# Kernel optimization log

Measured on AMD Instinct MI355X. Metric: run time of the kernel, lower is better.

Reference implementation:

```python
import jax, jax.numpy as jnp
import numpy as np

HEADS = 8
EPS = 1e-5


def setup_inputs() -> dict:
    key = jax.random.key(0)
    B, N, C = 32, 4096, 256
    headc = C // HEADS
    x = jax.random.normal(key, (B, N, C), dtype=jnp.float32)
    return {
        "x": x,
        "kln_weight": jnp.ones((HEADS, 1, headc), dtype=jnp.float32),
        "kln_bias": jnp.zeros((HEADS, 1, headc), dtype=jnp.float32),
        "vln_weight": jnp.ones((HEADS, 1, headc), dtype=jnp.float32),
        "vln_bias": jnp.zeros((HEADS, 1, headc), dtype=jnp.float32),
    }


def _ln(t, w, b, headc):
    # Faithful to the torch module: unbiased std (ddof=1), eps added to std (not var).
    m = jnp.mean(t, axis=-1, keepdims=True)
    d = t - m
    std = jnp.sqrt(jnp.sum(d * d, axis=-1, keepdims=True) / (headc - 1))
    return w * (d / (std + EPS)) + b


def reference(x, kln_weight, kln_bias, vln_weight, vln_bias):
    B, N, C = x.shape
    headc = C // HEADS
    # [B, H, N, D]
    qkv = x.reshape(B, N, HEADS, headc).transpose(0, 2, 1, 3)
    k = _ln(qkv, kln_weight, kln_bias, headc)
    v = _ln(qkv, vln_weight, vln_bias, headc)
    # k^T v : [B, H, D, D], scaled by 1/N
    kv = jnp.einsum("bhnd,bhne->bhde", k, v) / N
    # q (k^T v): [B, H, N, D]
    out = jnp.einsum("bhnd,bhde->bhne", qkv, kv)
    out = out.transpose(0, 2, 1, 3).reshape(B, N, C)
    return out + x
```

## Files before the change

kernel.cpp:

```cpp
#include <hip/hip_runtime.h>

#define H_ 8
#define D_ 32
#define B_ 32
#define N_ 4096
#define C_ 256
#define EPS_ 1e-5f

#define SLOT_ 1088

typedef __attribute__((ext_vector_type(8))) short bf16x8;
typedef __attribute__((ext_vector_type(4))) float f32x4;

__device__ __forceinline__ short f2bf(float f) {
    unsigned u = __builtin_bit_cast(unsigned, f);
    unsigned r = (u + 0x7FFFu + ((u >> 16) & 1u)) >> 16;
    return (short)r;
}
__device__ __forceinline__ float bf2f(short s) {
    return __builtin_bit_cast(float, ((unsigned)(unsigned short)s) << 16);
}

__device__ __forceinline__ int uidx(int r, int c) {
    return r * 40 + ((r >> 3) & 3) * 16 + c;
}

__global__ __launch_bounds__(256, 4)
void k1_skv(const float* __restrict__ x, float* __restrict__ Pws)
{
    __shared__ short ubuf[256 * 40 + 64];

    const int tid  = threadIdx.x;
    const int bh   = blockIdx.x >> 2;
    const int q4   = blockIdx.x & 3;
    const int b    = bh >> 3;
    const int h    = bh & 7;
    const int lane = tid & 63;
    const int wave = tid >> 6;
    const int g    = lane >> 4;
    const int cL   = lane & 15;

    f32x4 acc[2][2] = {};
    f32x4 tq[2] = {};

    bf16x8 ones;
    #pragma unroll
    for (int j = 0; j < 8; ++j) ones[j] = (short)0x3F80;

    const float* xbase = x + ((size_t)b * N_ + q4 * 1024 + tid) * C_ + h * D_;

    float4 xA[8], xB[8];
    #pragma unroll
    for (int c = 0; c < 8; ++c)
        xA[c] = reinterpret_cast<const float4*>(xbase)[c];

    auto body = [&](const float4 (&xr)[8], float4 (&nx)[8], int it, bool pf) {
        if (pf) {
            const float* p = xbase + (size_t)(it + 1) * 256 * C_;
            #pragma unroll
            for (int c = 0; c < 8; ++c)
                nx[c] = reinterpret_cast<const float4*>(p)[c];
        }

        float sum = 0.f, sq = 0.f;
        #pragma unroll
        for (int c = 0; c < 8; ++c) {
            const float4 a = xr[c];
            sum += a.x + a.y + a.z + a.w;
            sq = fmaf(a.x, a.x, fmaf(a.y, a.y, fmaf(a.z, a.z, fmaf(a.w, a.w, sq))));
        }
        const float m   = sum * (1.f / 32.f);
        const float ss  = fmaxf(sq - sum * m, 0.f);
        const float inv = 1.f / (sqrtf(ss * (1.f / 31.f)) + EPS_);

        {
            const int base = tid * 40 + ((tid >> 3) & 3) * 16;
            #pragma unroll
            for (int q = 0; q < 4; ++q) {
                const float4 a0 = xr[q * 2 + 0];
                const float4 a1 = xr[q * 2 + 1];
                bf16x8 wv;
                wv[0] = f2bf((a0.x - m) * inv); wv[1] = f2bf((a0.y - m) * inv);
                wv[2] = f2bf((a0.z - m) * inv); wv[3] = f2bf((a0.w - m) * inv);
                wv[4] = f2bf((a1.x - m) * inv); wv[5] = f2bf((a1.y - m) * inv);
                wv[6] = f2bf((a1.z - m) * inv); wv[7] = f2bf((a1.w - m) * inv);
                *reinterpret_cast<bf16x8*>(&ubuf[base + q * 8]) = wv;
            }
        }
        asm volatile("s_waitcnt lgkmcnt(0)" ::: "memory");

        #pragma unroll
        for (int ks = 0; ks < 2; ++ks) {
            const int R0 = wave * 64 + ks * 32 + 8 * g;
            bf16x8 F0, F1;
            #pragma unroll
            for (int j = 0; j < 8; ++j) {
                const int base = uidx(R0 + j, cL);
                F0[j] = ubuf[base];
                F1[j] = ubuf[base + 16];
            }
            tq[0] = __builtin_amdgcn_mfma_f32_16x16x32_bf16(ones, F0, tq[0], 0, 0, 0);
            tq[1] = __builtin_amdgcn_mfma_f32_16x16x32_bf16(ones, F1, tq[1], 0, 0, 0);
            acc[0][0] = __builtin_amdgcn_mfma_f32_16x16x32_bf16(F0, F0, acc[0][0], 0, 0, 0);
            acc[0][1] = __builtin_amdgcn_mfma_f32_16x16x32_bf16(F0, F1, acc[0][1], 0, 0, 0);
            acc[1][0] = __builtin_amdgcn_mfma_f32_16x16x32_bf16(F1, F0, acc[1][0], 0, 0, 0);
            acc[1][1] = __builtin_amdgcn_mfma_f32_16x16x32_bf16(F1, F1, acc[1][1], 0, 0, 0);
        }
    };

    body(xA, xB, 0, true);
    body(xB, xA, 1, true);
    body(xA, xB, 2, true);
    body(xB, xA, 3, false);

    __syncthreads();
    float* sred = reinterpret_cast<float*>(ubuf);
    {
        float* dst = sred + wave * 1024;
        #pragma unroll
        for (int ca = 0; ca < 2; ++ca)
            #pragma unroll
            for (int cb = 0; cb < 2; ++cb)
                #pragma unroll
                for (int r = 0; r < 4; ++r)
                    dst[(ca * 16 + g * 4 + r) * D_ + cb * 16 + cL] = acc[ca][cb][r];
    }
    if (lane < 16) {
        sred[4096 + wave * 32 + cL]      = tq[0][0];
        sred[4096 + wave * 32 + 16 + cL] = tq[1][0];
    }
    __syncthreads();

    float* slot = Pws + (size_t)blockIdx.x * SLOT_;
    {
        const float4 c0 = *reinterpret_cast<const float4*>(&sred[tid * 4]);
        const float4 c1 = *reinterpret_cast<const float4*>(&sred[1024 + tid * 4]);
        const float4 c2 = *reinterpret_cast<const float4*>(&sred[2048 + tid * 4]);
        const float4 c3 = *reinterpret_cast<const float4*>(&sred[3072 + tid * 4]);
        float4 o;
        o.x = c0.x + c1.x + c2.x + c3.x;
        o.y = c0.y + c1.y + c2.y + c3.y;
        o.z = c0.z + c1.z + c2.z + c3.z;
        o.w = c0.w + c1.w + c2.w + c3.w;
        *reinterpret_cast<float4*>(slot + tid * 4) = o;
    }
    if (tid < D_)
        slot[1024 + tid] = sred[4096 + tid] + sred[4096 + 32 + tid]
                         + sred[4096 + 64 + tid] + sred[4096 + 96 + tid];
}

__global__ __launch_bounds__(256, 4)
void k_red(const float* __restrict__ Pws,
           const float* __restrict__ kw, const float* __restrict__ kb,
           const float* __restrict__ vw, const float* __restrict__ vb,
           short* __restrict__ kvHi, short* __restrict__ kvLo)
{
    const int bh  = blockIdx.x;
    const int h   = bh & 7;
    const int tid = threadIdx.x;
    const int d   = tid >> 3;
    const int e0  = (tid & 7) * 4;

    const float* P0 = Pws + (size_t)(bh * 4 + 0) * SLOT_;
    const float* P1 = Pws + (size_t)(bh * 4 + 1) * SLOT_;
    const float* P2 = Pws + (size_t)(bh * 4 + 2) * SLOT_;
    const float* P3 = Pws + (size_t)(bh * 4 + 3) * SLOT_;
    const float invN = 1.f / (float)N_;

    const float4 s0 = *reinterpret_cast<const float4*>(P0 + d * D_ + e0);
    const float4 s1 = *reinterpret_cast<const float4*>(P1 + d * D_ + e0);
    const float4 s2 = *reinterpret_cast<const float4*>(P2 + d * D_ + e0);
    const float4 s3 = *reinterpret_cast<const float4*>(P3 + d * D_ + e0);
    float Sde[4] = { s0.x + s1.x + s2.x + s3.x, s0.y + s1.y + s2.y + s3.y,
                     s0.z + s1.z + s2.z + s3.z, s0.w + s1.w + s2.w + s3.w };

    const float Td  = P0[1024 + d] + P1[1024 + d] + P2[1024 + d] + P3[1024 + d];
    const float wkd = kw[h * D_ + d];
    const float bkd = kb[h * D_ + d];

    #pragma unroll
    for (int j = 0; j < 4; ++j) {
        const int e = e0 + j;
        const float Te  = P0[1024 + e] + P1[1024 + e] + P2[1024 + e] + P3[1024 + e];
        const float wve = vw[h * D_ + e];
        const float bve = vb[h * D_ + e];
        const float v = invN * (wkd * (wve * Sde[j] + bve * Td) + bkd * wve * Te)
                      + bkd * bve;
        const short hi = f2bf(v);
        const short lo = f2bf(v - bf2f(hi));
        const int hf  = e >> 4;
        const int l   = ((d >> 3) << 4) | (e & 15);
        const int idx = bh * 1024 + hf * 512 + l * 8 + (d & 7);
        kvHi[idx] = hi;
        kvLo[idx] = lo;
    }
}

__global__ __launch_bounds__(256, 2)
void k2_out(const float* __restrict__ x,
            const short* __restrict__ kvHi, const short* __restrict__ kvLo,
            float* __restrict__ out)
{
    __shared__ float xt[64][256];

    const int tid  = threadIdx.x;
    const int lane = tid & 63;
    const int w    = tid >> 6;
    const int g    = lane >> 4;
    const int cL   = lane & 15;
    const int r0   = blockIdx.x * 64;
    const int b    = blockIdx.x >> 6;
    const int wr   = w * 16;

    bf16x8 Bhi[16], Blo[16];
    #pragma unroll
    for (int h = 0; h < 8; ++h)
        #pragma unroll
        for (int hf = 0; hf < 2; ++hf) {
            const size_t off = (size_t)(b * H_ + h) * 1024 + hf * 512 + lane * 8;
            Bhi[h * 2 + hf] = *reinterpret_cast<const bf16x8*>(kvHi + off);
            Blo[h * 2 + hf] = *reinterpret_cast<const bf16x8*>(kvLo + off);
        }

    const float* gx = x + (size_t)(r0 + wr) * C_ + lane * 4;
    {
        float4 v[8];
        #pragma unroll
        for (int i = 0; i < 8; ++i)
            v[i] = *reinterpret_cast<const float4*>(gx + (size_t)i * C_);
        #pragma unroll
        for (int i = 0; i < 8; ++i)
            *reinterpret_cast<float4*>(&xt[wr + i][lane * 4]) = v[i];
        #pragma unroll
        for (int i = 0; i < 8; ++i)
            v[i] = *reinterpret_cast<const float4*>(gx + (size_t)(i + 8) * C_);
        #pragma unroll
        for (int i = 0; i < 8; ++i)
            *reinterpret_cast<float4*>(&xt[wr + 8 + i][lane * 4]) = v[i];
    }
    asm volatile("s_waitcnt lgkmcnt(0)" ::: "memory");
    __builtin_amdgcn_sched_barrier(0);

    const f32x4 zero = {0.f, 0.f, 0.f, 0.f};

    #pragma unroll
    for (int h = 0; h < 8; ++h) {
        const float4 a0 = *reinterpret_cast<const float4*>(&xt[wr + cL][h * 32 + 8 * g]);
        const float4 a1 = *reinterpret_cast<const float4*>(&xt[wr + cL][h * 32 + 8 * g + 4]);
        bf16x8 A;
        A[0] = f2bf(a0.x); A[1] = f2bf(a0.y); A[2] = f2bf(a0.z); A[3] = f2bf(a0.w);
        A[4] = f2bf(a1.x); A[5] = f2bf(a1.y); A[6] = f2bf(a1.z); A[7] = f2bf(a1.w);

        #pragma unroll
        for (int hf = 0; hf < 2; ++hf) {
            f32x4 Dv = __builtin_amdgcn_mfma_f32_16x16x32_bf16(A, Blo[h * 2 + hf], zero, 0, 0, 0);
            Dv = __builtin_amdgcn_mfma_f32_16x16x32_bf16(A, Bhi[h * 2 + hf], Dv, 0, 0, 0);
            const int col = h * 32 + hf * 16 + cL;
            #pragma unroll
            for (int r = 0; r < 4; ++r) {
                const int rr = wr + 4 * g + r;
                out[(size_t)(r0 + rr) * C_ + col] = Dv[r] + xt[rr][col];
            }
        }
    }
}

extern "C" void kernel_launch(void* const* d_in, const int* in_sizes, int n_in,
                              void* d_out, int out_size, void* d_ws, size_t ws_size,
                              hipStream_t stream)
{
    const float* x  = (const float*)d_in[0];
    const float* kw = (const float*)d_in[1];
    const float* kb = (const float*)d_in[2];
    const float* vw = (const float*)d_in[3];
    const float* vb = (const float*)d_in[4];
    float* outp = (float*)d_out;

    float* Pws  = (float*)d_ws;
    short* kvHi = (short*)(Pws + (size_t)1024 * SLOT_);
    short* kvLo = kvHi + (size_t)256 * 1024;

    k1_skv<<<dim3(B_ * H_ * 4), dim3(256), 0, stream>>>(x, Pws);
    k_red<<<dim3(B_ * H_), dim3(256), 0, stream>>>(Pws, kw, kb, vw, vb, kvHi, kvLo);
    k2_out<<<dim3(B_ * N_ / 64), dim3(256), 0, stream>>>(x, kvHi, kvLo, outp);
}
```

Measured before the change: 81.24 us.

## Fold residual into KV via identity, drop LDS staging in output kernel

Adds the identity matrix to the per-head KV matrix so the residual x is produced by the matmul itself, which lets the output kernel skip re-reading x for the add. The output kernel no longer stages x tiles in shared memory. It loads q and the KV fragments straight from global memory, software-pipelined two heads at a time, and swaps the MFMA operands so each lane writes a contiguous float4. Occupancy is raised to 4 blocks per SM. The cost is that the residual now passes through bf16 hi/lo precision on q, which may add error to the added x term.

```diff
diff --git a/kernel.cpp b/kernel.cpp
--- a/kernel.cpp
+++ b/kernel.cpp
@@ -184,8 +184,9 @@
         const float Te  = P0[1024 + e] + P1[1024 + e] + P2[1024 + e] + P3[1024 + e];
         const float wve = vw[h * D_ + e];
         const float bve = vb[h * D_ + e];
-        const float v = invN * (wkd * (wve * Sde[j] + bve * Td) + bkd * wve * Te)
-                      + bkd * bve;
+        float v = invN * (wkd * (wve * Sde[j] + bve * Td) + bkd * wve * Te)
+                + bkd * bve;
+        if (d == e) v += 1.0f;
         const short hi = f2bf(v);
         const short lo = f2bf(v - bf2f(hi));
         const int hf  = e >> 4;
@@ -196,73 +197,71 @@
     }
 }
 
-__global__ __launch_bounds__(256, 2)
+__global__ __launch_bounds__(256, 4)
 void k2_out(const float* __restrict__ x,
             const short* __restrict__ kvHi, const short* __restrict__ kvLo,
             float* __restrict__ out)
 {
-    __shared__ float xt[64][256];
-
     const int tid  = threadIdx.x;
     const int lane = tid & 63;
     const int w    = tid >> 6;
     const int g    = lane >> 4;
     const int cL   = lane & 15;
-    const int r0   = blockIdx.x * 64;
     const int b    = blockIdx.x >> 6;
-    const int wr   = w * 16;
-
-    bf16x8 Bhi[16], Blo[16];
-    #pragma unroll
-    for (int h = 0; h < 8; ++h)
-        #pragma unroll
-        for (int hf = 0; hf < 2; ++hf) {
-            const size_t off = (size_t)(b * H_ + h) * 1024 + hf * 512 + lane * 8;
-            Bhi[h * 2 + hf] = *reinterpret_cast<const bf16x8*>(kvHi + off);
-            Blo[h * 2 + hf] = *reinterpret_cast<const bf16x8*>(kvLo + off);
-        }
-
-    const float* gx = x + (size_t)(r0 + wr) * C_ + lane * 4;
-    {
-        float4 v[8];
-        #pragma unroll
-        for (int i = 0; i < 8; ++i)
-            v[i] = *reinterpret_cast<const float4*>(gx + (size_t)i * C_);
-        #pragma unroll
-        for (int i = 0; i < 8; ++i)
-            *reinterpret_cast<float4*>(&xt[wr + i][lane * 4]) = v[i];
-        #pragma unroll
-        for (int i = 0; i < 8; ++i)
-            v[i] = *reinterpret_cast<const float4*>(gx + (size_t)(i + 8) * C_);
-        #pragma unroll
-        for (int i = 0; i < 8; ++i)
-            *reinterpret_cast<float4*>(&xt[wr + 8 + i][lane * 4]) = v[i];
-    }
-    asm volatile("s_waitcnt lgkmcnt(0)" ::: "memory");
-    __builtin_amdgcn_sched_barrier(0);
+    const int row  = blockIdx.x * 64 + w * 16 + cL;
+
+    const float* xr   = x + (size_t)row * C_;
+    float*       orow = out + (size_t)row * C_;
+    const size_t fb   = (size_t)(b * H_) * 1024 + lane * 8;
 
     const f32x4 zero = {0.f, 0.f, 0.f, 0.f};
 
-    #pragma unroll
-    for (int h = 0; h < 8; ++h) {
-        const float4 a0 = *reinterpret_cast<const float4*>(&xt[wr + cL][h * 32 + 8 * g]);
-        const float4 a1 = *reinterpret_cast<const float4*>(&xt[wr + cL][h * 32 + 8 * g + 4]);
-        bf16x8 A;
-        A[0] = f2bf(a0.x); A[1] = f2bf(a0.y); A[2] = f2bf(a0.z); A[3] = f2bf(a0.w);
-        A[4] = f2bf(a1.x); A[5] = f2bf(a1.y); A[6] = f2bf(a1.z); A[7] = f2bf(a1.w);
-
-        #pragma unroll
-        for (int hf = 0; hf < 2; ++hf) {
-            f32x4 Dv = __builtin_amdgcn_mfma_f32_16x16x32_bf16(A, Blo[h * 2 + hf], zero, 0, 0, 0);
-            Dv = __builtin_amdgcn_mfma_f32_16x16x32_bf16(A, Bhi[h * 2 + hf], Dv, 0, 0, 0);
-            const int col = h * 32 + hf * 16 + cL;
-            #pragma unroll
-            for (int r = 0; r < 4; ++r) {
-                const int rr = wr + 4 * g + r;
-                out[(size_t)(r0 + rr) * C_ + col] = Dv[r] + xt[rr][col];
-            }
-        }
-    }
+    bf16x8 hA0, lA0, hA1, lA1, hB0, lB0, hB1, lB1;
+    float4 qA0, qA1, qB0, qB1;
+
+#define LOADH(H, h0, l0, h1, l1, q0, q1)                                      \
+    h0 = *reinterpret_cast<const bf16x8*>(kvHi + fb + (H) * 1024);            \
+    l0 = *reinterpret_cast<const bf16x8*>(kvLo + fb + (H) * 1024);            \
+    h1 = *reinterpret_cast<const bf16x8*>(kvHi + fb + (H) * 1024 + 512);      \
+    l1 = *reinterpret_cast<const bf16x8*>(kvLo + fb + (H) * 1024 + 512);      \
+    q0 = *reinterpret_cast<const float4*>(xr + (H) * 32 + 8 * g);             \
+    q1 = *reinterpret_cast<const float4*>(xr + (H) * 32 + 8 * g + 4);
+
+#define COMPUTE(H, h0, l0, h1, l1, q0, q1)                                    \
+    {                                                                         \
+        bf16x8 Qb;                                                            \
+        Qb[0] = f2bf(q0.x); Qb[1] = f2bf(q0.y);                               \
+        Qb[2] = f2bf(q0.z); Qb[3] = f2bf(q0.w);                               \
+        Qb[4] = f2bf(q1.x); Qb[5] = f2bf(q1.y);                               \
+        Qb[6] = f2bf(q1.z); Qb[7] = f2bf(q1.w);                               \
+        f32x4 Dv;                                                             \
+        Dv = __builtin_amdgcn_mfma_f32_16x16x32_bf16(l0, Qb, zero, 0, 0, 0);  \
+        Dv = __builtin_amdgcn_mfma_f32_16x16x32_bf16(h0, Qb, Dv,   0, 0, 0);  \
+        *reinterpret_cast<f32x4*>(orow + (H) * 32 + 4 * g) = Dv;              \
+        Dv = __builtin_amdgcn_mfma_f32_16x16x32_bf16(l1, Qb, zero, 0, 0, 0);  \
+        Dv = __builtin_amdgcn_mfma_f32_16x16x32_bf16(h1, Qb, Dv,   0, 0, 0);  \
+        *reinterpret_cast<f32x4*>(orow + (H) * 32 + 16 + 4 * g) = Dv;         \
+    }
+
+    LOADH(0, hA0, lA0, hA1, lA1, qA0, qA1)
+    LOADH(1, hB0, lB0, hB1, lB1, qB0, qB1)
+    COMPUTE(0, hA0, lA0, hA1, lA1, qA0, qA1)
+    LOADH(2, hA0, lA0, hA1, lA1, qA0, qA1)
+    COMPUTE(1, hB0, lB0, hB1, lB1, qB0, qB1)
+    LOADH(3, hB0, lB0, hB1, lB1, qB0, qB1)
+    COMPUTE(2, hA0, lA0, hA1, lA1, qA0, qA1)
+    LOADH(4, hA0, lA0, hA1, lA1, qA0, qA1)
+    COMPUTE(3, hB0, lB0, hB1, lB1, qB0, qB1)
+    LOADH(5, hB0, lB0, hB1, lB1, qB0, qB1)
+    COMPUTE(4, hA0, lA0, hA1, lA1, qA0, qA1)
+    LOADH(6, hA0, lA0, hA1, lA1, qA0, qA1)
+    COMPUTE(5, hB0, lB0, hB1, lB1, qB0, qB1)
+    LOADH(7, hB0, lB0, hB1, lB1, qB0, qB1)
+    COMPUTE(6, hA0, lA0, hA1, lA1, qA0, qA1)
+    COMPUTE(7, hB0, lB0, hB1, lB1, qB0, qB1)
+
+#undef LOADH
+#undef COMPUTE
 }
 
 extern "C" void kernel_launch(void* const* d_in, const int* in_sizes, int n_in,
```

After: 84.50 us. 1.04x slower.

## Cache normalized rows in bf16 and fold the residual into kv via identity

Applied to the files above, without the earlier changes.

The first kernel now also writes each row's normalized values as bf16, plus its mean and std, to a global workspace. The reduction kernel adds the identity to kv, so q·kv + q becomes q·(kv+I), and it stores the column sums of that matrix. The output kernel rebuilds the result as sdev·(u·kv') + mean·colsum, so it reads half-size bf16 data instead of fp32 x and stages kv in LDS. In exchange the first kernel writes an extra intermediate, so total memory traffic may not drop. The residual now passes through bf16-rounded values, which loses accuracy, and the output stores are now per-row 16-byte chunks instead of coalesced row writes.

```diff
diff --git a/kernel.cpp b/kernel.cpp
--- a/kernel.cpp
+++ b/kernel.cpp
@@ -26,7 +26,8 @@
 }
 
 __global__ __launch_bounds__(256, 4)
-void k1_skv(const float* __restrict__ x, float* __restrict__ Pws)
+void k1_skv(const float* __restrict__ x, float* __restrict__ Pws,
+            short* __restrict__ ug, float2* __restrict__ msg)
 {
     __shared__ short ubuf[256 * 40 + 64];
 
@@ -69,10 +70,13 @@
             sum += a.x + a.y + a.z + a.w;
             sq = fmaf(a.x, a.x, fmaf(a.y, a.y, fmaf(a.z, a.z, fmaf(a.w, a.w, sq))));
         }
-        const float m   = sum * (1.f / 32.f);
-        const float ss  = fmaxf(sq - sum * m, 0.f);
-        const float inv = 1.f / (sqrtf(ss * (1.f / 31.f)) + EPS_);
-
+        const float m    = sum * (1.f / 32.f);
+        const float ss   = fmaxf(sq - sum * m, 0.f);
+        const float sdev = sqrtf(ss * (1.f / 31.f)) + EPS_;
+        const float inv  = 1.0f / sdev;
+
+        const size_t nrow = (size_t)bh * N_ + (size_t)q4 * 1024 + it * 256 + tid;
+        short* up = ug + nrow * 32;
         {
             const int base = tid * 40 + ((tid >> 3) & 3) * 16;
             #pragma unroll
@@ -85,8 +89,10 @@
                 wv[4] = f2bf((a1.x - m) * inv); wv[5] = f2bf((a1.y - m) * inv);
                 wv[6] = f2bf((a1.z - m) * inv); wv[7] = f2bf((a1.w - m) * inv);
                 *reinterpret_cast<bf16x8*>(&ubuf[base + q * 8]) = wv;
+                *reinterpret_cast<bf16x8*>(up + q * 8) = wv;
             }
         }
+        msg[nrow] = make_float2(m, sdev);
         asm volatile("s_waitcnt lgkmcnt(0)" ::: "memory");
 
         #pragma unroll
@@ -153,8 +159,11 @@
 void k_red(const float* __restrict__ Pws,
            const float* __restrict__ kw, const float* __restrict__ kb,
            const float* __restrict__ vw, const float* __restrict__ vb,
-           short* __restrict__ kvHi, short* __restrict__ kvLo)
+           short* __restrict__ kvHi, short* __restrict__ kvLo,
+           float* __restrict__ tp)
 {
+    __shared__ float kvm[1024];
+
     const int bh  = blockIdx.x;
     const int h   = bh & 7;
     const int tid = threadIdx.x;
@@ -184,8 +193,10 @@
         const float Te  = P0[1024 + e] + P1[1024 + e] + P2[1024 + e] + P3[1024 + e];
         const float wve = vw[h * D_ + e];
         const float bve = vb[h * D_ + e];
-        const float v = invN * (wkd * (wve * Sde[j] + bve * Td) + bkd * wve * Te)
-                      + bkd * bve;
+        float v = invN * (wkd * (wve * Sde[j] + bve * Td) + bkd * wve * Te)
+                + bkd * bve;
+        if (d == e) v += 1.0f;
+        kvm[d * 32 + e] = v;
         const short hi = f2bf(v);
         const short lo = f2bf(v - bf2f(hi));
         const int hf  = e >> 4;
@@ -194,73 +205,76 @@
         kvHi[idx] = hi;
         kvLo[idx] = lo;
     }
-}
-
-__global__ __launch_bounds__(256, 2)
-void k2_out(const float* __restrict__ x,
+    __syncthreads();
+    if (tid < 32) {
+        float s = 0.f;
+        #pragma unroll 8
+        for (int dd = 0; dd < 32; ++dd) s += kvm[dd * 32 + tid];
+        tp[bh * 32 + tid] = s;
+    }
+}
+
+__global__ __launch_bounds__(256, 4)
+void k2_out(const short* __restrict__ ug, const float2* __restrict__ msg,
             const short* __restrict__ kvHi, const short* __restrict__ kvLo,
-            float* __restrict__ out)
+            const float* __restrict__ tp, float* __restrict__ out)
 {
-    __shared__ float xt[64][256];
+    __shared__ short kvL[16384];
+    __shared__ float tpL[256];
 
     const int tid  = threadIdx.x;
     const int lane = tid & 63;
     const int w    = tid >> 6;
     const int g    = lane >> 4;
     const int cL   = lane & 15;
-    const int r0   = blockIdx.x * 64;
     const int b    = blockIdx.x >> 6;
-    const int wr   = w * 16;
-
-    bf16x8 Bhi[16], Blo[16];
+    const int n    = (blockIdx.x & 63) * 64 + w * 16 + cL;
+
+    {
+        const short* srcH = kvHi + (size_t)b * 8192;
+        const short* srcL = kvLo + (size_t)b * 8192;
+        #pragma unroll
+        for (int i = 0; i < 4; ++i) {
+            const int o = (tid + i * 256) * 8;
+            *reinterpret_cast<bf16x8*>(&kvL[o]) =
+                *reinterpret_cast<const bf16x8*>(srcH + o);
+            *reinterpret_cast<bf16x8*>(&kvL[8192 + o]) =
+                *reinterpret_cast<const bf16x8*>(srcL + o);
+        }
+        tpL[tid] = tp[b * 256 + tid];
+    }
+
+    bf16x8 A[8];
+    float2 ms[8];
+    const short* up = ug + ((size_t)(b * 8) * N_ + n) * 32 + g * 8;
     #pragma unroll
     for (int h = 0; h < 8; ++h)
+        A[h] = *reinterpret_cast<const bf16x8*>(up + (size_t)h * N_ * 32);
+    #pragma unroll
+    for (int h = 0; h < 8; ++h)
+        ms[h] = msg[(size_t)(b * 8 + h) * N_ + n];
+
+    __syncthreads();
+
+    float* orow = out + ((size_t)b * N_ + n) * C_;
+    const f32x4 zero = {0.f, 0.f, 0.f, 0.f};
+
+    #pragma unroll
+    for (int h = 0; h < 8; ++h) {
         #pragma unroll
         for (int hf = 0; hf < 2; ++hf) {
-            const size_t off = (size_t)(b * H_ + h) * 1024 + hf * 512 + lane * 8;
-            Bhi[h * 2 + hf] = *reinterpret_cast<const bf16x8*>(kvHi + off);
-            Blo[h * 2 + hf] = *reinterpret_cast<const bf16x8*>(kvLo + off);
-        }
-
-    const float* gx = x + (size_t)(r0 + wr) * C_ + lane * 4;
-    {
-        float4 v[8];
-        #pragma unroll
-        for (int i = 0; i < 8; ++i)
-            v[i] = *reinterpret_cast<const float4*>(gx + (size_t)i * C_);
-        #pragma unroll
-        for (int i = 0; i < 8; ++i)
-            *reinterpret_cast<float4*>(&xt[wr + i][lane * 4]) = v[i];
-        #pragma unroll
-        for (int i = 0; i < 8; ++i)
-            v[i] = *reinterpret_cast<const float4*>(gx + (size_t)(i + 8) * C_);
-        #pragma unroll
-        for (int i = 0; i < 8; ++i)
-            *reinterpret_cast<float4*>(&xt[wr + 8 + i][lane * 4]) = v[i];
-    }
-    asm volatile("s_waitcnt lgkmcnt(0)" ::: "memory");
-    __builtin_amdgcn_sched_barrier(0);
-
-    const f32x4 zero = {0.f, 0.f, 0.f, 0.f};
-
-    #pragma unroll
-    for (int h = 0; h < 8; ++h) {
-        const float4 a0 = *reinterpret_cast<const float4*>(&xt[wr + cL][h * 32 + 8 * g]);
-        const float4 a1 = *reinterpret_cast<const float4*>(&xt[wr + cL][h * 32 + 8 * g + 4]);
-        bf16x8 A;
-        A[0] = f2bf(a0.x); A[1] = f2bf(a0.y); A[2] = f2bf(a0.z); A[3] = f2bf(a0.w);
-        A[4] = f2bf(a1.x); A[5] = f2bf(a1.y); A[6] = f2bf(a1.z); A[7] = f2bf(a1.w);
-
-        #pragma unroll
-        for (int hf = 0; hf < 2; ++hf) {
-            f32x4 Dv = __builtin_amdgcn_mfma_f32_16x16x32_bf16(A, Blo[h * 2 + hf], zero, 0, 0, 0);
-            Dv = __builtin_amdgcn_mfma_f32_16x16x32_bf16(A, Bhi[h * 2 + hf], Dv, 0, 0, 0);
-            const int col = h * 32 + hf * 16 + cL;
-            #pragma unroll
-            for (int r = 0; r < 4; ++r) {
-                const int rr = wr + 4 * g + r;
-                out[(size_t)(r0 + rr) * C_ + col] = Dv[r] + xt[rr][col];
-            }
+            const int si = h * 1024 + hf * 512 + lane * 8;
+            const bf16x8 hi = *reinterpret_cast<const bf16x8*>(&kvL[si]);
+            const bf16x8 lo = *reinterpret_cast<const bf16x8*>(&kvL[8192 + si]);
+            f32x4 Dv;
+            Dv = __builtin_amdgcn_mfma_f32_16x16x32_bf16(lo, A[h], zero, 0, 0, 0);
+            Dv = __builtin_amdgcn_mfma_f32_16x16x32_bf16(hi, A[h], Dv,   0, 0, 0);
+            const f32x4 t4 = *reinterpret_cast<const f32x4*>(&tpL[h * 32 + hf * 16 + 4 * g]);
+            f32x4 o;
+            #pragma unroll
+            for (int c = 0; c < 4; ++c)
+                o[c] = fmaf(ms[h].y, Dv[c], ms[h].x * t4[c]);
+            *reinterpret_cast<f32x4*>(orow + h * 32 + hf * 16 + 4 * g) = o;
         }
     }
 }
@@ -276,11 +290,14 @@
     const float* vb = (const float*)d_in[4];
     float* outp = (float*)d_out;
 
-    float* Pws  = (float*)d_ws;
-    short* kvHi = (short*)(Pws + (size_t)1024 * SLOT_);
-    short* kvLo = kvHi + (size_t)256 * 1024;
-
-    k1_skv<<<dim3(B_ * H_ * 4), dim3(256), 0, stream>>>(x, Pws);
-    k_red<<<dim3(B_ * H_), dim3(256), 0, stream>>>(Pws, kw, kb, vw, vb, kvHi, kvLo);
-    k2_out<<<dim3(B_ * N_ / 64), dim3(256), 0, stream>>>(x, kvHi, kvLo, outp);
-}
+    float*  Pws  = (float*)d_ws;
+    short*  kvHi = (short*)(Pws + (size_t)1024 * SLOT_);
+    short*  kvLo = kvHi + (size_t)256 * 1024;
+    float*  tp   = (float*)(kvLo + (size_t)256 * 1024);
+    short*  ug   = (short*)(tp + (size_t)256 * 32);
+    float2* msg  = (float2*)(ug + (size_t)256 * N_ * 32);
+
+    k1_skv<<<dim3(B_ * H_ * 4), dim3(256), 0, stream>>>(x, Pws, ug, msg);
+    k_red<<<dim3(B_ * H_), dim3(256), 0, stream>>>(Pws, kw, kb, vw, vb, kvHi, kvLo, tp);
+    k2_out<<<dim3(B_ * N_ / 64), dim3(256), 0, stream>>>(ug, msg, kvHi, kvLo, tp, outp);
+}
```

Measured after the change: 113.5 us. 39.7% more time.
